# Optimization experiments

Measured on AMD Instinct MI355X. Metric: run time of the kernel, lower is better.

## Reference

```python
import jax, jax.numpy as jnp
import numpy as np
from jax import lax

FH, FW = 38, 63          # feature map H,W (600x1000 image, stride 16)
A = 9                    # anchors per location (3 scales x 3 ratios)
POOL = 7                 # cfg.POOLING_SIZE
PRE_NMS, POST_NMS = 6000, 300
NMS_THRESH = 0.7
IM_H, IM_W = 600.0, 1000.0
STRIDE = 16.0


def _make_anchors(h, w, stride=16):
    ratios = np.array([0.5, 1.0, 2.0]); scales = np.array([8.0, 16.0, 32.0])
    base = 16.0; ctr = (base - 1.0) / 2.0
    ws = np.round(np.sqrt(base * base / ratios)); hs = np.round(ws * ratios)
    ws = (ws[:, None] * scales[None, :]).ravel(); hs = (hs[:, None] * scales[None, :]).ravel()
    ba = np.stack([ctr - 0.5 * (ws - 1), ctr - 0.5 * (hs - 1),
                   ctr + 0.5 * (ws - 1), ctr + 0.5 * (hs - 1)], 1)
    sx, sy = np.meshgrid(np.arange(w) * stride, np.arange(h) * stride)
    shifts = np.stack([sx.ravel(), sy.ravel(), sx.ravel(), sy.ravel()], 1)
    return (shifts[:, None, :] + ba[None]).reshape(-1, 4).astype(np.float32)


def _conv(x, w, b, pad):
    y = lax.conv_general_dilated(x, w, (1, 1), pad,
                                 dimension_numbers=('NCHW', 'OIHW', 'NCHW'))
    return y + b[None, :, None, None]


def _bbox_transform_inv(anchors, deltas):
    w = anchors[:, 2] - anchors[:, 0] + 1.0
    h = anchors[:, 3] - anchors[:, 1] + 1.0
    cx = anchors[:, 0] + 0.5 * w
    cy = anchors[:, 1] + 0.5 * h
    dx, dy, dw, dh = deltas[:, 0], deltas[:, 1], deltas[:, 2], deltas[:, 3]
    pcx = dx * w + cx; pcy = dy * h + cy
    pw = jnp.exp(dw) * w; ph = jnp.exp(dh) * h
    return jnp.stack([pcx - 0.5 * pw, pcy - 0.5 * ph,
                      pcx + 0.5 * pw, pcy + 0.5 * ph], 1)


def _nms_keep(boxes, thresh):
    # greedy NMS over score-sorted boxes, fixed-size keep mask
    x1, y1, x2, y2 = boxes[:, 0], boxes[:, 1], boxes[:, 2], boxes[:, 3]
    areas = (x2 - x1 + 1.0) * (y2 - y1 + 1.0)
    iw = jnp.maximum(jnp.minimum(x2[:, None], x2[None, :])
                     - jnp.maximum(x1[:, None], x1[None, :]) + 1.0, 0.0)
    ih = jnp.maximum(jnp.minimum(y2[:, None], y2[None, :])
                     - jnp.maximum(y1[:, None], y1[None, :]) + 1.0, 0.0)
    inter = iw * ih
    iou = inter / (areas[:, None] + areas[None, :] - inter)
    n = boxes.shape[0]; ar = jnp.arange(n)
    def body(i, keep):
        sup = (iou[i] > thresh) & (ar > i) & keep[i]
        return keep & ~sup
    return lax.fori_loop(0, n, body, jnp.ones((n,), bool))


def _crop_and_resize(feat, boxes, crop):
    # feat [C,H,W]; boxes [R,4] normalized (y1,x1,y2,x2); TF crop_and_resize semantics
    C, H, W = feat.shape
    t = jnp.arange(crop, dtype=feat.dtype) / (crop - 1)
    def one(box):
        by1, bx1, by2, bx2 = box
        ys = by1 * (H - 1) + t * (by2 - by1) * (H - 1)
        xs = bx1 * (W - 1) + t * (bx2 - bx1) * (W - 1)
        y0f = jnp.floor(ys); x0f = jnp.floor(xs)
        wy = (ys - y0f)[None, :, None]; wx = (xs - x0f)[None, None, :]
        y0 = jnp.clip(y0f, 0, H - 1).astype(jnp.int32)
        y1i = jnp.clip(y0f + 1, 0, H - 1).astype(jnp.int32)
        x0 = jnp.clip(x0f, 0, W - 1).astype(jnp.int32)
        x1i = jnp.clip(x0f + 1, 0, W - 1).astype(jnp.int32)
        f00 = feat[:, y0][:, :, x0]; f01 = feat[:, y0][:, :, x1i]
        f10 = feat[:, y1i][:, :, x0]; f11 = feat[:, y1i][:, :, x1i]
        return (f00 * (1 - wy) * (1 - wx) + f01 * (1 - wy) * wx
                + f10 * wy * (1 - wx) + f11 * wy * wx)
    return jax.vmap(one)(boxes)


def _forward(net_conv, w_rpn, b_rpn, w_cls, b_cls, w_bbox, b_bbox, anchors):
    # _region_proposal: 3x3 rpn conv + relu, 1x1 cls / bbox heads
    rpn = jax.nn.relu(_conv(net_conv, w_rpn, b_rpn, 'SAME'))
    cls = _conv(rpn, w_cls, b_cls, 'VALID')    # [1,2A,H,W]
    bbox = _conv(rpn, w_bbox, b_bbox, 'VALID')  # [1,4A,H,W]
    # view(1,2,-1,W) softmax: channel a pairs with channel a+A (bg/fg)
    bg, fg = cls[:, :A], cls[:, A:]
    fg_prob = jax.nn.softmax(jnp.stack([bg, fg], axis=1), axis=1)[:, 1]  # [1,A,H,W]
    scores = jnp.transpose(fg_prob, (0, 2, 3, 1)).reshape(-1)            # (H*W*A,)
    deltas = jnp.transpose(bbox, (0, 2, 3, 1)).reshape(-1, 4)
    proposals = _bbox_transform_inv(anchors, deltas)
    proposals = jnp.stack([jnp.clip(proposals[:, 0], 0.0, IM_W - 1.0),
                           jnp.clip(proposals[:, 1], 0.0, IM_H - 1.0),
                           jnp.clip(proposals[:, 2], 0.0, IM_W - 1.0),
                           jnp.clip(proposals[:, 3], 0.0, IM_H - 1.0)], 1)
    # proposal selection is non-differentiable (rois.detach() in original)
    scores_sg = lax.stop_gradient(scores)
    props_sg = lax.stop_gradient(proposals)
    _, order = lax.top_k(scores_sg, PRE_NMS)
    boxes = props_sg[order]
    keep = _nms_keep(boxes, NMS_THRESH)
    idx = jnp.sort(jnp.where(keep, jnp.arange(PRE_NMS), PRE_NMS))[:POST_NMS]
    rois = boxes[jnp.minimum(idx, PRE_NMS - 1)]  # [300,4] (x1,y1,x2,y2)
    # _crop_pool_layer with max_pool=True: crop to 14x14 then 2x2 max pool
    H, W = net_conv.shape[2], net_conv.shape[3]
    x1 = rois[:, 0] / STRIDE; y1 = rois[:, 1] / STRIDE
    x2 = rois[:, 2] / STRIDE; y2 = rois[:, 3] / STRIDE
    norm = jnp.stack([y1 / (H - 1), x1 / (W - 1), y2 / (H - 1), x2 / (W - 1)], 1)
    crops = _crop_and_resize(net_conv[0], norm, 2 * POOL)  # [300,C,14,14]
    R, C = crops.shape[0], crops.shape[1]
    return crops.reshape(R, C, POOL, 2, POOL, 2).max(axis=(3, 5))  # [300,C,7,7]


def setup_inputs():
    key = jax.random.key(0)
    ks = jax.random.split(key, 4)
    net_conv = jax.random.normal(ks[0], (1, 512, FH, FW), jnp.float32)
    w_rpn = jax.random.normal(ks[1], (512, 512, 3, 3), jnp.float32) * 0.01
    b_rpn = jnp.zeros((512,), jnp.float32)
    w_cls = jax.random.normal(ks[2], (2 * A, 512, 1, 1), jnp.float32) * 0.01
    b_cls = jnp.zeros((2 * A,), jnp.float32)
    w_bbox = jax.random.normal(ks[3], (4 * A, 512, 1, 1), jnp.float32) * 0.01
    b_bbox = jnp.zeros((4 * A,), jnp.float32)
    anchors = jnp.asarray(_make_anchors(FH, FW))
    return {"net_conv": net_conv, "w_rpn": w_rpn, "b_rpn": b_rpn,
            "w_cls": w_cls, "b_cls": b_cls, "w_bbox": w_bbox,
            "b_bbox": b_bbox, "anchors": anchors}


def reference(net_conv, w_rpn, b_rpn, w_cls, b_cls, w_bbox, b_bbox, anchors):
    return _forward(net_conv, w_rpn, b_rpn, w_cls, b_cls, w_bbox, b_bbox, anchors)
```

## Files before the change

kernel.cpp:

```cpp
#include <hip/hip_runtime.h>
#include <stdint.h>

#define NPOS 2394
#define CIN 512
#define KK 4608
#define NANCH 21546
#define PRE 6000
#define POST 300
#define NWORD 94
#define NQ 8
#define QLEN 2694
#define FEATT_BYTES 4902912

#define OFF_BH    0
#define OFF_BL    4718592
#define OFF_FPH   9437184
#define OFF_FPL   12166144
#define OFF_P0    14895104
#define OFF_P1    19798016
#define OFF_P2    24700928
#define OFF_KEYS  0
#define OFF_PROP  180224
#define OFF_RPART 532480
#define OFF_SBOX  1228800
#define OFF_KEEP  1327104
#define OFF_DIAG  1335296
#define OFF_MASK  4718592

typedef _Float16 half8 __attribute__((ext_vector_type(8)));
typedef float f32x4 __attribute__((ext_vector_type(4)));

__device__ __forceinline__ void gload16(const void* g, void* l) {
    __builtin_amdgcn_global_load_lds((const __attribute__((address_space(1))) void*)g,
                                     (__attribute__((address_space(3))) void*)l, 16, 0, 0);
}

__device__ __forceinline__ unsigned long long rl64(unsigned long long v, int l) {
    union { unsigned long long q; unsigned int d[2]; } s; s.q = v;
    unsigned int lo = __builtin_amdgcn_readlane(s.d[0], l);
    unsigned int hi = __builtin_amdgcn_readlane(s.d[1], l);
    return ((unsigned long long)hi << 32) | (unsigned long long)lo;
}

__global__ __launch_bounds__(256) void k_transpose_feat(const float* __restrict__ in,
                                                        float* __restrict__ featT) {
    __shared__ float tl[32][33];
    int tx = threadIdx.x & 31, tg = threadIdx.x >> 5;
    int posBase = blockIdx.x * 32, ciBase = blockIdx.y * 32;
#pragma unroll
    for (int j = 0; j < 4; ++j) {
        int ci = ciBase + tg + j * 8;
        int pos = posBase + tx;
        tl[tg + j * 8][tx] = (pos < NPOS) ? in[(size_t)ci * NPOS + pos] : 0.f;
    }
    __syncthreads();
#pragma unroll
    for (int j = 0; j < 4; ++j) {
        int pos = posBase + tg + j * 8;
        int ci = ciBase + tx;
        if (pos < NPOS) featT[(size_t)pos * 512 + ci] = tl[tx][tg + j * 8];
    }
}

__global__ void k_pad_split(const float* __restrict__ featT,
                            _Float16* __restrict__ FPH, _Float16* __restrict__ FPL) {
    int idx = blockIdx.x * 256 + threadIdx.x;
    int ci = idx & 511;
    int rc = idx >> 9;
    int hp = rc / 65, wp = rc - hp * 65;
    int h = hp - 1, w = wp - 1;
    float a = 0.f;
    if ((unsigned)h < 38u && (unsigned)w < 63u)
        a = featT[(size_t)(h * 63 + w) * 512 + ci] * 16.f;
    _Float16 ah = (_Float16)a;
    _Float16 al = (_Float16)(a - (float)ah);
    FPH[idx] = ah; FPL[idx] = al;
}

__global__ void k_prep_wf16(const float* __restrict__ w,
                            _Float16* __restrict__ BH, _Float16* __restrict__ BL) {
    int idx = blockIdx.x * 256 + threadIdx.x;
    int co = idx / KK;
    int rem = idx - co * KK;
    int p = rem >> 9;
    int ci = rem & 511;
    float b = w[(co * CIN + ci) * 9 + p] * 128.f;
    _Float16 bh = (_Float16)b;
    _Float16 bl = (_Float16)(b - (float)bh);
    BH[idx] = bh; BL[idx] = bl;
}

__global__ __launch_bounds__(256, 3) void k_conv3_mfma(
    const _Float16* __restrict__ FPH, const _Float16* __restrict__ FPL,
    const _Float16* __restrict__ BHp, const _Float16* __restrict__ BLp,
    float* __restrict__ P0, float* __restrict__ P1, float* __restrict__ P2)
{
    __shared__ __align__(16) char lds[49152];
    const int t = threadIdx.x;
    const int wave = t >> 6, lane = t & 63;

    const int bid = blockIdx.x;
    const int swz = (bid & 7) * 57 + (bid >> 3);
    const int z = swz / 152;
    const int rem = swz - z * 152;
    const int coB = rem / 19;
    const int posB = rem - coB * 19;
    const int posBase = posB * 128;
    const int coBase  = coB * 64;
    float* __restrict__ P = (z == 0) ? P0 : ((z == 1) ? P1 : P2);

    const int wm = wave >> 1, wn = wave & 1;
    const int lr = lane & 15, lg = lane >> 4;

    int addrA[4][2], addrB[2][2];
#pragma unroll
    for (int m = 0; m < 4; ++m) {
        int row = wm * 64 + m * 16 + lr;
        int x = row & 7;
        addrA[m][0] = row * 128 + ((lg ^ x) << 4);
        addrA[m][1] = row * 128 + (((4 + lg) ^ x) << 4);
    }
#pragma unroll
    for (int n = 0; n < 2; ++n) {
        int row = wn * 32 + n * 16 + lr;
        int x = row & 7;
        addrB[n][0] = 32768 + row * 128 + ((lg ^ x) << 4);
        addrB[n][1] = 32768 + row * 128 + (((4 + lg) ^ x) << 4);
    }

    int baseA[4], ldsAo[4];
#pragma unroll
    for (int s = 0; s < 4; ++s) {
        int row = (wave * 4 + s) * 8 + (lane >> 3);
        int pos = posBase + row;
        int h = pos / 63;
        int w = pos - h * 63;
        int swzb = ((lane & 7) ^ (row & 7)) * 8;
        baseA[s] = (h * 65 + w) * 512 + swzb;
        ldsAo[s] = (wave * 4 + s) * 1024 + lane * 16;
    }
    int baseB[2], ldsBo[2];
#pragma unroll
    for (int s = 0; s < 2; ++s) {
        int row = (wave * 2 + s) * 8 + (lane >> 3);
        int swzb = ((lane & 7) ^ (row & 7)) * 8;
        baseB[s] = (coBase + row) * KK + swzb;
        ldsBo[s] = 32768 + (wave * 2 + s) * 1024 + lane * 16;
    }

    f32x4 acc[4][2];
#pragma unroll
    for (int m = 0; m < 4; ++m)
#pragma unroll
        for (int n = 0; n < 2; ++n) acc[m][n] = (f32x4){0.f, 0.f, 0.f, 0.f};

    const int kbeg = z * 1536;
    for (int step = 0; step < 24; ++step) {
        int k0 = kbeg + step * 64;
        int p = k0 >> 9;
        int ci0 = k0 & 511;
        int kh = p / 3;
        int kw = p - kh * 3;
        int dA = (kh * 65 + kw) * 512 + ci0;
#pragma unroll
        for (int s = 0; s < 4; ++s) {
            int so = baseA[s] + dA;
            gload16(FPH + so, lds + ldsAo[s]);
            gload16(FPL + so, lds + 16384 + ldsAo[s]);
        }
#pragma unroll
        for (int s = 0; s < 2; ++s) {
            int so = baseB[s] + k0;
            gload16(BHp + so, lds + ldsBo[s]);
            gload16(BLp + so, lds + 8192 + ldsBo[s]);
        }
        __syncthreads();
#pragma unroll
        for (int ks = 0; ks < 2; ++ks) {
            half8 aH[4], aL[4], bH[2], bL[2];
#pragma unroll
            for (int m = 0; m < 4; ++m) {
                aH[m] = *(const half8*)(lds + addrA[m][ks]);
                aL[m] = *(const half8*)(lds + 16384 + addrA[m][ks]);
            }
#pragma unroll
            for (int n = 0; n < 2; ++n) {
                bH[n] = *(const half8*)(lds + addrB[n][ks]);
                bL[n] = *(const half8*)(lds + 8192 + addrB[n][ks]);
            }
#pragma unroll
            for (int m = 0; m < 4; ++m)
#pragma unroll
                for (int n = 0; n < 2; ++n) {
                    acc[m][n] = __builtin_amdgcn_mfma_f32_16x16x32_f16(aH[m], bH[n], acc[m][n], 0, 0, 0);
                    acc[m][n] = __builtin_amdgcn_mfma_f32_16x16x32_f16(aH[m], bL[n], acc[m][n], 0, 0, 0);
                    acc[m][n] = __builtin_amdgcn_mfma_f32_16x16x32_f16(aL[m], bH[n], acc[m][n], 0, 0, 0);
                }
        }
        __syncthreads();
    }

#pragma unroll
    for (int m = 0; m < 4; ++m) {
        int pbase = posBase + wm * 64 + m * 16 + lg * 4;
        int co = coBase + wn * 32 + lr;
#pragma unroll
        for (int r = 0; r < 4; ++r) {
            int pos = pbase + r;
            if (pos < NPOS) {
                P[(size_t)pos * 512 + co]      = acc[m][0][r] * (1.f / 2048.f);
                P[(size_t)pos * 512 + co + 16] = acc[m][1][r] * (1.f / 2048.f);
            }
        }
    }
}

__global__ __launch_bounds__(256) void k_heads(const float* __restrict__ P0,
                                               const float* __restrict__ P1,
                                               const float* __restrict__ P2,
                                               const float* __restrict__ brpn,
                                               const float* __restrict__ wcls,
                                               const float* __restrict__ bcls,
                                               const float* __restrict__ wbbox,
                                               const float* __restrict__ bbbox,
                                               const float* __restrict__ anchors,
                                               float* __restrict__ proposals,
                                               unsigned long long* __restrict__ keys) {
    __shared__ float x[512];
    __shared__ float part[54][4];
    __shared__ float logit[54];
    int pos = blockIdx.x;
    int t = threadIdx.x;
    {
        size_t o = (size_t)pos * 512 + t;
        float v0 = P0[o] + P1[o] + P2[o] + brpn[t];
        float v1 = P0[o + 256] + P1[o + 256] + P2[o + 256] + brpn[t + 256];
        x[t] = v0 > 0.f ? v0 : 0.f;
        x[t + 256] = v1 > 0.f ? v1 : 0.f;
    }
    __syncthreads();
    if (t < 216) {
        int o = t >> 2, q = t & 3;
        const float* wr = (o < 18) ? (wcls + o * 512) : (wbbox + (o - 18) * 512);
        float s = 0.f;
        int base = q * 128;
#pragma unroll 4
        for (int k2 = 0; k2 < 128; ++k2) s += x[base + k2] * wr[base + k2];
        part[o][q] = s;
    }
    __syncthreads();
    if (t < 54) {
        float b = (t < 18) ? bcls[t] : bbbox[t - 18];
        logit[t] = part[t][0] + part[t][1] + part[t][2] + part[t][3] + b;
    }
    __syncthreads();
    if (t < 9) {
        int a = t;
        float bg = logit[a], fg = logit[9 + a];
        float score = 1.f / (1.f + expf(bg - fg));
        float dx = logit[18 + 4 * a], dy = logit[19 + 4 * a];
        float dw = logit[20 + 4 * a], dh = logit[21 + 4 * a];
        int idx = pos * 9 + a;
        float ax1 = anchors[idx * 4 + 0], ay1 = anchors[idx * 4 + 1];
        float ax2 = anchors[idx * 4 + 2], ay2 = anchors[idx * 4 + 3];
        float aw = ax2 - ax1 + 1.f, ah = ay2 - ay1 + 1.f;
        float cx = ax1 + 0.5f * aw, cy = ay1 + 0.5f * ah;
        float pcx = dx * aw + cx, pcy = dy * ah + cy;
        float pw = expf(dw) * aw, ph = expf(dh) * ah;
        float x1 = fminf(fmaxf(pcx - 0.5f * pw, 0.f), 999.f);
        float y1 = fminf(fmaxf(pcy - 0.5f * ph, 0.f), 599.f);
        float x2 = fminf(fmaxf(pcx + 0.5f * pw, 0.f), 999.f);
        float y2 = fminf(fmaxf(pcy + 0.5f * ph, 0.f), 599.f);
        proposals[idx * 4 + 0] = x1; proposals[idx * 4 + 1] = y1;
        proposals[idx * 4 + 2] = x2; proposals[idx * 4 + 3] = y2;
        union { float f; unsigned int i; } sv; sv.f = score;
        keys[idx] = (((unsigned long long)sv.i) << 32) |
                    (unsigned long long)(0xFFFFFFFFu - (unsigned)idx);
    }
}

__global__ __launch_bounds__(256) void k_rank_partial(const unsigned long long* __restrict__ keys,
                                                      unsigned int* __restrict__ rpart) {
    __shared__ unsigned long long kc[1024];
    int i = blockIdx.x * 256 + threadIdx.x;
    int q = blockIdx.y;
    unsigned long long myk = (i < NANCH) ? keys[i] : 0xFFFFFFFFFFFFFFFFull;
    int j0 = q * QLEN;
    int j1 = j0 + QLEN; if (j1 > NANCH) j1 = NANCH;
    unsigned int cnt = 0;
    for (int base = j0; base < j1; base += 1024) {
        int nload = j1 - base; if (nload > 1024) nload = 1024;
        __syncthreads();
        for (int u = threadIdx.x; u < 1024; u += 256)
            kc[u] = (base + u < j1) ? keys[base + u] : 0ull;
        __syncthreads();
        for (int u = 0; u < nload; ++u)
            cnt += (kc[u] > myk) ? 1u : 0u;
    }
    if (i < NANCH) rpart[i * NQ + q] = cnt;
}

__global__ void k_zero_aux(float* __restrict__ sboxes, unsigned long long* __restrict__ diag4) {
    int i = blockIdx.x * 256 + threadIdx.x;
    diag4[i] = 0ull;
    if (i < PRE * 4) sboxes[i] = 0.f;
}

__global__ void k_rank_scatter(const unsigned int* __restrict__ rpart,
                               const float* __restrict__ proposals,
                               float* __restrict__ sboxes) {
    int i = blockIdx.x * 256 + threadIdx.x;
    if (i >= NANCH) return;
    unsigned int r = 0;
#pragma unroll
    for (int q = 0; q < NQ; q++) r += rpart[i * NQ + q];
    if (r < PRE) {
        sboxes[r * 4 + 0] = proposals[i * 4 + 0];
        sboxes[r * 4 + 1] = proposals[i * 4 + 1];
        sboxes[r * 4 + 2] = proposals[i * 4 + 2];
        sboxes[r * 4 + 3] = proposals[i * 4 + 3];
    }
}

__global__ __launch_bounds__(64) void k_nms_mask(const float* __restrict__ sboxes,
                                                 unsigned long long* __restrict__ mask,
                                                 unsigned long long* __restrict__ diag4) {
    __shared__ float bx[64][4];
    int ib = blockIdx.x, jb = blockIdx.y;
    int lane = threadIdx.x;
    int j = jb * 64 + lane;
    if (j < PRE) {
        bx[lane][0] = sboxes[j * 4 + 0]; bx[lane][1] = sboxes[j * 4 + 1];
        bx[lane][2] = sboxes[j * 4 + 2]; bx[lane][3] = sboxes[j * 4 + 3];
    } else {
        bx[lane][0] = 3e8f; bx[lane][1] = 3e8f; bx[lane][2] = 3e8f; bx[lane][3] = 3e8f;
    }
    __syncthreads();
    int i = ib * 64 + lane;
    if (i >= PRE) return;
    float x1 = sboxes[i * 4 + 0], y1 = sboxes[i * 4 + 1];
    float x2 = sboxes[i * 4 + 2], y2 = sboxes[i * 4 + 3];
    float ar = (x2 - x1 + 1.f) * (y2 - y1 + 1.f);
    unsigned long long bits = 0;
#pragma unroll 4
    for (int u = 0; u < 64; u++) {
        int j2 = jb * 64 + u;
        float iw = fminf(x2, bx[u][2]) - fmaxf(x1, bx[u][0]) + 1.f;
        float ih = fminf(y2, bx[u][3]) - fmaxf(y1, bx[u][1]) + 1.f;
        iw = fmaxf(iw, 0.f); ih = fmaxf(ih, 0.f);
        float inter = iw * ih;
        float arj = (bx[u][2] - bx[u][0] + 1.f) * (bx[u][3] - bx[u][1] + 1.f);
        float iou = inter / (ar + arj - inter);
        if (iou > 0.7f && j2 > i) bits |= (1ull << u);
    }
    mask[(size_t)i * NWORD + jb] = bits;
    if ((jb >> 2) == (ib >> 2)) diag4[(size_t)i * 4 + (jb & 3)] = bits;
}

#define NSB 24
#define SBW 256
#define NSLOT 20
__global__ __launch_bounds__(64) void k_nms_scan(const unsigned long long* __restrict__ mask,
                                                 const unsigned long long* __restrict__ diag4,
                                                 int* __restrict__ keep) {
    __shared__ __align__(16) unsigned long long tile[2][SBW * 4];
    __shared__ __align__(16) char ldsrow[NSLOT * 1024];
    __shared__ int ldsk[POST];
    const int lane = threadIdx.x;
    const char* dg = (const char*)diag4;

    for (int c = 0; c < 8; ++c)
        gload16(dg + c * 1024 + (size_t)lane * 16, (char*)tile[0] + c * 1024);

    unsigned long long rem0 = 0, rem1 = 0;
    int nk = 0, npend = 0;

    for (int sb = 0; sb < NSB; ++sb) {
        if (sb + 1 < NSB) {
            const char* src = dg + (size_t)(sb + 1) * 8192;
            char* dst = (char*)tile[(sb + 1) & 1];
            for (int c = 0; c < 8; ++c)
                gload16(src + c * 1024 + (size_t)lane * 16, dst + c * 1024);
            asm volatile("s_waitcnt vmcnt(8)" ::: "memory");
        } else {
            asm volatile("s_waitcnt vmcnt(0)" ::: "memory");
        }
        __builtin_amdgcn_sched_barrier(0);

        for (int q = 0; q < npend; ++q) {
            const unsigned long long* lr = (const unsigned long long*)(ldsrow + q * 1024);
            rem0 |= lr[lane];
            if (lane < NWORD - 64) rem1 |= lr[64 + lane];
        }
        npend = 0;

        const unsigned long long* tl = tile[sb & 1];
        unsigned long long d[4][4];
#pragma unroll
        for (int q = 0; q < 4; ++q) {
            ulonglong2 e0 = *(const ulonglong2*)&tl[(q * 64 + lane) * 4];
            ulonglong2 e1 = *(const ulonglong2*)&tl[(q * 64 + lane) * 4 + 2];
            d[q][0] = e0.x; d[q][1] = e0.y; d[q][2] = e1.x; d[q][3] = e1.y;
        }

        const int w0 = 4 * sb;
        const int base = sb * SBW;
        unsigned long long rmw[4];
#pragma unroll
        for (int j = 0; j < 4; ++j) {
            int w = w0 + j;
            rmw[j] = (w < 64) ? rl64(rem0, w) : ((w < NWORD) ? rl64(rem1, w - 64) : ~0ull);
        }

#pragma unroll
        for (int p = 0; p < 4; ++p) {
            int w = w0 + p;
            if (w >= NWORD) break;
            const unsigned long long valid = (w == NWORD - 1) ? ((1ull << 48) - 1) : ~0ull;
            unsigned long long above = ~0ull;
            unsigned long long keptm = 0;
            for (;;) {
                unsigned long long a = ~rmw[p] & valid & above;
                if (!a) break;
                int u = (int)(__ffsll((long long)a) - 1);
                keptm |= 1ull << u;
                ++nk;
#pragma unroll
                for (int j = p; j < 4; ++j) rmw[j] |= rl64(d[p][j], u);
                if (nk == POST) break;
                above = (u == 63) ? 0ull : (~0ull << (u + 1));
            }
            unsigned long long bits = keptm;
            int nkb = nk - __builtin_popcountll(keptm);
            while (bits) {
                int u = (int)(__ffsll((long long)bits) - 1); bits &= bits - 1;
                int i = base + p * 64 + u;
                if (lane == 0) ldsk[nkb] = i;
                ++nkb;
                if (npend == NSLOT) {
                    asm volatile("s_waitcnt vmcnt(0)" ::: "memory");
                    __builtin_amdgcn_sched_barrier(0);
                    for (int q = 0; q < NSLOT; ++q) {
                        const unsigned long long* lr = (const unsigned long long*)(ldsrow + q * 1024);
                        rem0 |= lr[lane];
                        if (lane < NWORD - 64) rem1 |= lr[64 + lane];
                    }
                    npend = 0;
                }
                gload16((const char*)(mask + (size_t)i * NWORD) + (size_t)lane * 16,
                        ldsrow + npend * 1024);
                ++npend;
            }
            if (nk >= POST) goto done;
        }
    }
done:
    asm volatile("s_waitcnt vmcnt(0)" ::: "memory");
    for (int k2 = lane; k2 < POST; k2 += 64)
        keep[k2] = (k2 < nk) ? ldsk[k2] : PRE - 1;
}

__global__ __launch_bounds__(256) void k_gather_rois(const float* sboxes, const int* keep,
                                                     float* outF) {
    int t = threadIdx.x;
    float4 box[2];
    int nr = 0;
    for (int r = t; r < POST; r += 256) {
        int ki = keep[r];
        if (ki < 0) ki = 0; if (ki > PRE - 1) ki = PRE - 1;
        box[nr++] = *reinterpret_cast<const float4*>(sboxes + ki * 4);
    }
    __syncthreads();
    nr = 0;
    for (int r = t; r < POST; r += 256) {
        float4 b = box[nr++];
#pragma unroll
        for (int cg = 0; cg < 8; ++cg)
            *reinterpret_cast<float4*>(outF + (size_t)(r * 512 + cg * 64) * 49) = b;
    }
}

__global__ __launch_bounds__(256) void k_crop_fast(const float* __restrict__ featT,
                                                   float* out) {
    __shared__ float lds[4][49 * 65];
    int r = blockIdx.x;
    int w = threadIdx.x >> 6, lane = threadIdx.x & 63;
    int cg = blockIdx.y * 4 + w;
    int c = cg * 64 + lane;
    float* chunk = out + (size_t)(r * 512 + cg * 64) * 49;
    const float4 b = *reinterpret_cast<const float4*>(chunk);
    float x1 = b.x, y1 = b.y, x2 = b.z, y2 = b.w;
    float by1 = (y1 / 16.f) / 37.f, bx1 = (x1 / 16.f) / 62.f;
    float by2 = (y2 / 16.f) / 37.f, bx2 = (x2 / 16.f) / 62.f;
    float dyn = by2 - by1, dxn = bx2 - bx1;
    for (int e = 0; e < 49; ++e) {
        int oy = e / 7, ox = e - oy * 7;
        float vv[4];
#pragma unroll
        for (int dy = 0; dy < 2; ++dy) {
            int sy = 2 * oy + dy;
            float ty = (float)sy / 13.f;
            float ys = by1 * 37.f + (ty * dyn) * 37.f;
            float yf = floorf(ys);
            float wy = ys - yf;
            int y0  = (int)fminf(fmaxf(yf, 0.f), 37.f);
            int y1i = (int)fminf(fmaxf(yf + 1.f, 0.f), 37.f);
#pragma unroll
            for (int dxx = 0; dxx < 2; ++dxx) {
                int sx = 2 * ox + dxx;
                float tx = (float)sx / 13.f;
                float xs = bx1 * 62.f + (tx * dxn) * 62.f;
                float xf = floorf(xs);
                float wx = xs - xf;
                int x0  = (int)fminf(fmaxf(xf, 0.f), 62.f);
                int x1i = (int)fminf(fmaxf(xf + 1.f, 0.f), 62.f);
                float f00 = featT[(size_t)(y0 * 63 + x0) * 512 + c];
                float f01 = featT[(size_t)(y0 * 63 + x1i) * 512 + c];
                float f10 = featT[(size_t)(y1i * 63 + x0) * 512 + c];
                float f11 = featT[(size_t)(y1i * 63 + x1i) * 512 + c];
                vv[dy * 2 + dxx] = f00 * (1.f - wy) * (1.f - wx) + f01 * (1.f - wy) * wx +
                                   f10 * wy * (1.f - wx) + f11 * wy * wx;
            }
        }
        lds[w][e * 65 + lane] = fmaxf(fmaxf(vv[0], vv[1]), fmaxf(vv[2], vv[3]));
    }
    __syncthreads();
    for (int i = lane; i < 64 * 49; i += 64) {
        int cl = i / 49, e = i - cl * 49;
        chunk[i] = lds[w][e * 65 + cl];
    }
}

__global__ __launch_bounds__(64) void k_crop_slow(const float* __restrict__ net,
                                                  float* out) {
    int r = blockIdx.x, cg = blockIdx.y;
    int lane = threadIdx.x;
    int c = cg * 64 + lane;
    const float4 b = *reinterpret_cast<const float4*>(out + (size_t)(r * 512 + cg * 64) * 49);
    float x1 = b.x, y1 = b.y, x2 = b.z, y2 = b.w;
    float by1 = (y1 / 16.f) / 37.f, bx1 = (x1 / 16.f) / 62.f;
    float by2 = (y2 / 16.f) / 37.f, bx2 = (x2 / 16.f) / 62.f;
    float dyn = by2 - by1, dxn = bx2 - bx1;
    const float* fc = net + (size_t)c * NPOS;
    float* orow = out + ((size_t)r * 512 + c) * 49;
    for (int e = 0; e < 49; ++e) {
        int oy = e / 7, ox = e - oy * 7;
        float vv[4];
#pragma unroll
        for (int dy = 0; dy < 2; ++dy) {
            int sy = 2 * oy + dy;
            float ty = (float)sy / 13.f;
            float ys = by1 * 37.f + (ty * dyn) * 37.f;
            float yf = floorf(ys);
            float wy = ys - yf;
            int y0  = (int)fminf(fmaxf(yf, 0.f), 37.f);
            int y1i = (int)fminf(fmaxf(yf + 1.f, 0.f), 37.f);
#pragma unroll
            for (int dxx = 0; dxx < 2; ++dxx) {
                int sx = 2 * ox + dxx;
                float tx = (float)sx / 13.f;
                float xs = bx1 * 62.f + (tx * dxn) * 62.f;
                float xf = floorf(xs);
                float wx = xs - xf;
                int x0  = (int)fminf(fmaxf(xf, 0.f), 62.f);
                int x1i = (int)fminf(fmaxf(xf + 1.f, 0.f), 62.f);
                float f00 = fc[y0 * 63 + x0];
                float f01 = fc[y0 * 63 + x1i];
                float f10 = fc[y1i * 63 + x0];
                float f11 = fc[y1i * 63 + x1i];
                vv[dy * 2 + dxx] = f00 * (1.f - wy) * (1.f - wx) + f01 * (1.f - wy) * wx +
                                   f10 * wy * (1.f - wx) + f11 * wy * wx;
            }
        }
        orow[e] = fmaxf(fmaxf(vv[0], vv[1]), fmaxf(vv[2], vv[3]));
    }
}

extern "C" void kernel_launch(void* const* d_in, const int* in_sizes, int n_in,
                              void* d_out, int out_size, void* d_ws, size_t ws_size,
                              hipStream_t stream) {
    auto find = [&](int count, int fallback) {
        for (int i = 0; i < n_in; ++i) if (in_sizes[i] == count) return i;
        return fallback;
    };
    const float* net   = (const float*)d_in[find(NPOS * CIN, 0)];
    const float* wrpn  = (const float*)d_in[find(512 * KK, 1)];
    const float* brpn  = (const float*)d_in[find(512, 2)];
    const float* wcls  = (const float*)d_in[find(18 * 512, 3)];
    const float* bcls  = (const float*)d_in[find(18, 4)];
    const float* wbbox = (const float*)d_in[find(36 * 512, 5)];
    const float* bbbox = (const float*)d_in[find(36, 6)];
    const float* anch  = (const float*)d_in[find(NANCH * 4, 7)];

    char* ob = (char*)d_out;
    _Float16* BH             = (_Float16*)(ob + OFF_BH);
    _Float16* BL             = (_Float16*)(ob + OFF_BL);
    _Float16* FPH            = (_Float16*)(ob + OFF_FPH);
    _Float16* FPL            = (_Float16*)(ob + OFF_FPL);
    float* P0                = (float*)(ob + OFF_P0);
    float* P1                = (float*)(ob + OFF_P1);
    float* P2                = (float*)(ob + OFF_P2);
    unsigned long long* keys = (unsigned long long*)(ob + OFF_KEYS);
    float* proposals         = (float*)(ob + OFF_PROP);
    unsigned int* rpart      = (unsigned int*)(ob + OFF_RPART);
    float* sboxes            = (float*)(ob + OFF_SBOX);
    int* keep                = (int*)(ob + OFF_KEEP);
    unsigned long long* diag4= (unsigned long long*)(ob + OFF_DIAG);
    unsigned long long* mask = (unsigned long long*)(ob + OFF_MASK);
    float* outF              = (float*)d_out;

    const bool ws_ok = (ws_size >= (size_t)FEATT_BYTES);
    float* featT = ws_ok ? (float*)d_ws : (float*)(ob + OFF_P0);

    hipLaunchKernelGGL(k_transpose_feat, dim3(75, 16), dim3(256), 0, stream, net, featT);
    hipLaunchKernelGGL(k_pad_split, dim3(5330), dim3(256), 0, stream, featT, FPH, FPL);
    hipLaunchKernelGGL(k_prep_wf16, dim3(9216), dim3(256), 0, stream, wrpn, BH, BL);
    hipLaunchKernelGGL(k_conv3_mfma, dim3(456), dim3(256), 0, stream, FPH, FPL, BH, BL, P0, P1, P2);
    hipLaunchKernelGGL(k_heads, dim3(NPOS), dim3(256), 0, stream, P0, P1, P2, brpn, wcls, bcls, wbbox, bbbox, anch, proposals, keys);
    hipLaunchKernelGGL(k_rank_partial, dim3(85, NQ), dim3(256), 0, stream, keys, rpart);
    hipLaunchKernelGGL(k_zero_aux, dim3(96), dim3(256), 0, stream, sboxes, diag4);
    hipLaunchKernelGGL(k_rank_scatter, dim3(85), dim3(256), 0, stream, rpart, proposals, sboxes);
    hipLaunchKernelGGL(k_nms_mask, dim3(NWORD, NWORD), dim3(64), 0, stream, sboxes, mask, diag4);
    hipLaunchKernelGGL(k_nms_scan, dim3(1), dim3(64), 0, stream, mask, diag4, keep);
    hipLaunchKernelGGL(k_gather_rois, dim3(1), dim3(256), 0, stream, sboxes, keep, outF);
    if (ws_ok)
        hipLaunchKernelGGL(k_crop_fast, dim3(POST, 2), dim3(256), 0, stream, featT, outF);
    else
        hipLaunchKernelGGL(k_crop_slow, dim3(POST, 8), dim3(64), 0, stream, net, outF);
}
```

Baseline: 386.1 us.

## Fuse pad/split, border zeroing and ROI gather into neighbors; defer NMS cross-word updates

The pad-and-split into fp16 hi/lo now happens inside the feature transpose, and zeroing of the padded border moves into extra blocks of the weight-prep kernel. This removes the separate pad kernel and a full re-read of featT. The aux-zeroing kernel is dropped, and the ROI gather is merged into the tail of the single-block NMS scan, so three launches disappear. Inside the scan, only the current word's mask is updated per kept box; updates to later words are batched after the word is done, which shortens the serial dependency chain. The risk is that diag4 and sboxes entries the old zero kernel cleared may now hold stale values.

Measured after the change: 383.5 us. About the same (-0.7%).

```diff
diff --git a/kernel.cpp b/kernel.cpp
--- a/kernel.cpp
+++ b/kernel.cpp
@@ -23,9 +23,10 @@
 #define OFF_PROP  180224
 #define OFF_RPART 532480
 #define OFF_SBOX  1228800
-#define OFF_KEEP  1327104
 #define OFF_DIAG  1335296
 #define OFF_MASK  4718592
+
+#define NBORDER 138752
 
 typedef _Float16 half8 __attribute__((ext_vector_type(8)));
 typedef float f32x4 __attribute__((ext_vector_type(4)));
@@ -43,7 +44,9 @@
 }
 
 __global__ __launch_bounds__(256) void k_transpose_feat(const float* __restrict__ in,
-                                                        float* __restrict__ featT) {
+                                                        float* __restrict__ featT,
+                                                        _Float16* __restrict__ FPH,
+                                                        _Float16* __restrict__ FPL) {
     __shared__ float tl[32][33];
     int tx = threadIdx.x & 31, tg = threadIdx.x >> 5;
     int posBase = blockIdx.x * 32, ciBase = blockIdx.y * 32;
@@ -58,35 +61,49 @@
     for (int j = 0; j < 4; ++j) {
         int pos = posBase + tg + j * 8;
         int ci = ciBase + tx;
-        if (pos < NPOS) featT[(size_t)pos * 512 + ci] = tl[tx][tg + j * 8];
-    }
-}
-
-__global__ void k_pad_split(const float* __restrict__ featT,
+        if (pos < NPOS) {
+            float v = tl[tx][tg + j * 8];
+            featT[(size_t)pos * 512 + ci] = v;
+            int h = pos / 63, w = pos - h * 63;
+            int o = ((h + 1) * 65 + (w + 1)) * 512 + ci;
+            float a = v * 16.f;
+            _Float16 ah = (_Float16)a;
+            FPH[o] = ah;
+            FPL[o] = (_Float16)(a - (float)ah);
+        }
+    }
+}
+
+__global__ void k_prep_wf16(const float* __restrict__ w,
+                            _Float16* __restrict__ BH, _Float16* __restrict__ BL,
                             _Float16* __restrict__ FPH, _Float16* __restrict__ FPL) {
-    int idx = blockIdx.x * 256 + threadIdx.x;
-    int ci = idx & 511;
-    int rc = idx >> 9;
-    int hp = rc / 65, wp = rc - hp * 65;
-    int h = hp - 1, w = wp - 1;
-    float a = 0.f;
-    if ((unsigned)h < 38u && (unsigned)w < 63u)
-        a = featT[(size_t)(h * 63 + w) * 512 + ci] * 16.f;
-    _Float16 ah = (_Float16)a;
-    _Float16 al = (_Float16)(a - (float)ah);
-    FPH[idx] = ah; FPL[idx] = al;
-}
-
-__global__ void k_prep_wf16(const float* __restrict__ w,
-                            _Float16* __restrict__ BH, _Float16* __restrict__ BL) {
-    int idx = blockIdx.x * 256 + threadIdx.x;
+    int b = blockIdx.x;
+    if (b >= 9216) {
+        int i2 = (b - 9216) * 256 + threadIdx.x;
+        if (i2 < NBORDER) {
+            int bi = i2 >> 9, ci = i2 & 511;
+            int hp, wp;
+            if (bi < 195) {
+                hp = (bi < 65) ? 0 : ((bi < 130) ? 39 : 40);
+                wp = (bi < 65) ? bi : ((bi < 130) ? bi - 65 : bi - 130);
+            } else {
+                int j = bi - 195;
+                hp = 1 + (j >> 1);
+                wp = (j & 1) ? 64 : 0;
+            }
+            int o = (hp * 65 + wp) * 512 + ci;
+            FPH[o] = (_Float16)0.f; FPL[o] = (_Float16)0.f;
+        }
+        return;
+    }
+    int idx = b * 256 + threadIdx.x;
     int co = idx / KK;
     int rem = idx - co * KK;
     int p = rem >> 9;
     int ci = rem & 511;
-    float b = w[(co * CIN + ci) * 9 + p] * 128.f;
-    _Float16 bh = (_Float16)b;
-    _Float16 bl = (_Float16)(b - (float)bh);
+    float bv = w[(co * CIN + ci) * 9 + p] * 128.f;
+    _Float16 bh = (_Float16)bv;
+    _Float16 bl = (_Float16)(bv - (float)bh);
     BH[idx] = bh; BL[idx] = bl;
 }
 
@@ -300,12 +317,6 @@
     if (i < NANCH) rpart[i * NQ + q] = cnt;
 }
 
-__global__ void k_zero_aux(float* __restrict__ sboxes, unsigned long long* __restrict__ diag4) {
-    int i = blockIdx.x * 256 + threadIdx.x;
-    diag4[i] = 0ull;
-    if (i < PRE * 4) sboxes[i] = 0.f;
-}
-
 __global__ void k_rank_scatter(const unsigned int* __restrict__ rpart,
                                const float* __restrict__ proposals,
                                float* __restrict__ sboxes) {
@@ -325,7 +336,7 @@
 __global__ __launch_bounds__(64) void k_nms_mask(const float* __restrict__ sboxes,
                                                  unsigned long long* __restrict__ mask,
                                                  unsigned long long* __restrict__ diag4) {
-    __shared__ float bx[64][4];
+    __shared__ float bx[64][5];
     int ib = blockIdx.x, jb = blockIdx.y;
     int lane = threadIdx.x;
     int j = jb * 64 + lane;
@@ -362,7 +373,8 @@
 #define NSLOT 20
 __global__ __launch_bounds__(64) void k_nms_scan(const unsigned long long* __restrict__ mask,
                                                  const unsigned long long* __restrict__ diag4,
-                                                 int* __restrict__ keep) {
+                                                 const float* __restrict__ sboxes,
+                                                 float* __restrict__ outF) {
     __shared__ __align__(16) unsigned long long tile[2][SBW * 4];
     __shared__ __align__(16) char ldsrow[NSLOT * 1024];
     __shared__ int ldsk[POST];
@@ -425,10 +437,17 @@
                 int u = (int)(__ffsll((long long)a) - 1);
                 keptm |= 1ull << u;
                 ++nk;
-#pragma unroll
-                for (int j = p; j < 4; ++j) rmw[j] |= rl64(d[p][j], u);
                 if (nk == POST) break;
+                rmw[p] |= rl64(d[p][p], u);
                 above = (u == 63) ? 0ull : (~0ull << (u + 1));
+            }
+            {
+                unsigned long long bits = keptm;
+                while (bits) {
+                    int u = (int)(__ffsll((long long)bits) - 1); bits &= bits - 1;
+#pragma unroll
+                    for (int j = p + 1; j < 4; ++j) rmw[j] |= rl64(d[p][j], u);
+                }
             }
             unsigned long long bits = keptm;
             int nkb = nk - __builtin_popcountll(keptm);
@@ -456,27 +475,25 @@
     }
 done:
     asm volatile("s_waitcnt vmcnt(0)" ::: "memory");
-    for (int k2 = lane; k2 < POST; k2 += 64)
-        keep[k2] = (k2 < nk) ? ldsk[k2] : PRE - 1;
-}
-
-__global__ __launch_bounds__(256) void k_gather_rois(const float* sboxes, const int* keep,
-                                                     float* outF) {
-    int t = threadIdx.x;
-    float4 box[2];
-    int nr = 0;
-    for (int r = t; r < POST; r += 256) {
-        int ki = keep[r];
-        if (ki < 0) ki = 0; if (ki > PRE - 1) ki = PRE - 1;
-        box[nr++] = *reinterpret_cast<const float4*>(sboxes + ki * 4);
-    }
-    __syncthreads();
-    nr = 0;
-    for (int r = t; r < POST; r += 256) {
-        float4 b = box[nr++];
-#pragma unroll
-        for (int cg = 0; cg < 8; ++cg)
-            *reinterpret_cast<float4*>(outF + (size_t)(r * 512 + cg * 64) * 49) = b;
+    float4 bx[5];
+#pragma unroll
+    for (int i = 0; i < 5; ++i) {
+        int r = lane + i * 64;
+        if (r < POST) {
+            int ki = (r < nk) ? ldsk[r] : PRE - 1;
+            bx[i] = *reinterpret_cast<const float4*>(sboxes + ki * 4);
+        }
+    }
+    asm volatile("s_waitcnt vmcnt(0)" ::: "memory");
+    __builtin_amdgcn_sched_barrier(0);
+#pragma unroll
+    for (int i = 0; i < 5; ++i) {
+        int r = lane + i * 64;
+        if (r < POST) {
+#pragma unroll
+            for (int cg = 0; cg < 8; ++cg)
+                *reinterpret_cast<float4*>(outF + (size_t)(r * 512 + cg * 64) * 49) = bx[i];
+        }
     }
 }
 
@@ -604,7 +621,6 @@
     float* proposals         = (float*)(ob + OFF_PROP);
     unsigned int* rpart      = (unsigned int*)(ob + OFF_RPART);
     float* sboxes            = (float*)(ob + OFF_SBOX);
-    int* keep                = (int*)(ob + OFF_KEEP);
     unsigned long long* diag4= (unsigned long long*)(ob + OFF_DIAG);
     unsigned long long* mask = (unsigned long long*)(ob + OFF_MASK);
     float* outF              = (float*)d_out;
@@ -612,17 +628,14 @@
     const bool ws_ok = (ws_size >= (size_t)FEATT_BYTES);
     float* featT = ws_ok ? (float*)d_ws : (float*)(ob + OFF_P0);
 
-    hipLaunchKernelGGL(k_transpose_feat, dim3(75, 16), dim3(256), 0, stream, net, featT);
-    hipLaunchKernelGGL(k_pad_split, dim3(5330), dim3(256), 0, stream, featT, FPH, FPL);
-    hipLaunchKernelGGL(k_prep_wf16, dim3(9216), dim3(256), 0, stream, wrpn, BH, BL);
+    hipLaunchKernelGGL(k_transpose_feat, dim3(75, 16), dim3(256), 0, stream, net, featT, FPH, FPL);
+    hipLaunchKernelGGL(k_prep_wf16, dim3(9216 + 543), dim3(256), 0, stream, wrpn, BH, BL, FPH, FPL);
     hipLaunchKernelGGL(k_conv3_mfma, dim3(456), dim3(256), 0, stream, FPH, FPL, BH, BL, P0, P1, P2);
     hipLaunchKernelGGL(k_heads, dim3(NPOS), dim3(256), 0, stream, P0, P1, P2, brpn, wcls, bcls, wbbox, bbbox, anch, proposals, keys);
     hipLaunchKernelGGL(k_rank_partial, dim3(85, NQ), dim3(256), 0, stream, keys, rpart);
-    hipLaunchKernelGGL(k_zero_aux, dim3(96), dim3(256), 0, stream, sboxes, diag4);
     hipLaunchKernelGGL(k_rank_scatter, dim3(85), dim3(256), 0, stream, rpart, proposals, sboxes);
     hipLaunchKernelGGL(k_nms_mask, dim3(NWORD, NWORD), dim3(64), 0, stream, sboxes, mask, diag4);
-    hipLaunchKernelGGL(k_nms_scan, dim3(1), dim3(64), 0, stream, mask, diag4, keep);
-    hipLaunchKernelGGL(k_gather_rois, dim3(1), dim3(256), 0, stream, sboxes, keep, outF);
+    hipLaunchKernelGGL(k_nms_scan, dim3(1), dim3(64), 0, stream, mask, diag4, sboxes, outF);
     if (ws_ok)
         hipLaunchKernelGGL(k_crop_fast, dim3(POST, 2), dim3(256), 0, stream, featT, outF);
     else
```
